# Optimization experiments

Measured on AMD Instinct MI355X. Metric: run time of the kernel, lower is better.

## Reference

```python
import jax, jax.numpy as jnp
import numpy as np

N_FIELDS = 26
VOCAB = 100000
EMBED = 16
BATCH = 16384
K = 16
N = N_FIELDS * EMBED  # 416


def setup_inputs() -> dict:
    key = jax.random.key(0)
    k1, k2, k3, k4, k5 = jax.random.split(key, 5)
    X = jax.random.randint(k1, (BATCH, N_FIELDS), 0, VOCAB, dtype=jnp.int64)
    tables = jax.random.normal(k2, (N_FIELDS, VOCAB, EMBED), dtype=jnp.float32) * 0.01
    W = jax.random.normal(k3, (N, 1), dtype=jnp.float32) * 0.05
    b = jax.random.normal(k4, (1,), dtype=jnp.float32)
    v = jax.random.normal(k5, (N, K), dtype=jnp.float32) * 0.05
    return {"X": X, "tables": tables, "W": W, "b": b, "v": v}


def reference(X, tables, W, b, v):
    # per-field gather: tables[f, X[:, f]] -> [B, F, E]
    emb = jax.vmap(lambda t, idx: t[idx], in_axes=(0, 1), out_axes=1)(tables, X)
    all_emb = emb.reshape(emb.shape[0], -1)  # [B, n] concat over fields
    linear_part = all_emb @ W + b  # [B, 1]
    xv = all_emb @ v               # [B, k]
    square_of_sum = xv * xv
    sum_of_square = (all_emb * all_emb) @ (v * v)
    interaction = 0.5 * jnp.sum(square_of_sum - sum_of_square, axis=-1, keepdims=True)
    return jax.nn.sigmoid(linear_part + interaction)
```

## Files before the change

kernel.cpp:

```cpp
#include <hip/hip_runtime.h>
#include <math.h>

#define NF 26
#define VOCAB 100000
#define EMB 16
#define BATCH 16384
#define KD 16
#define NTOT (NF * EMB)
#define VSTRIDE 20

__global__ __launch_bounds__(256, 4) void fm_kernel(
    const int* __restrict__ X, const float* __restrict__ tables,
    const float* __restrict__ W, const float* __restrict__ bptr,
    const float* __restrict__ v, float* __restrict__ out) {
    __shared__ float vL[NTOT * VSTRIDE];
    __shared__ float2 wvs[NTOT];

    const int tid = threadIdx.x;

    for (int t = tid; t < NTOT * KD; t += 256) {
        int n = t >> 4, k = t & 15;
        vL[n * VSTRIDE + k] = v[t];
    }
    for (int n = tid; n < NTOT; n += 256) {
        const float* vr = v + n * KD;
        float s = 0.f;
#pragma unroll
        for (int k = 0; k < KD; ++k) s = fmaf(vr[k], vr[k], s);
        wvs[n] = make_float2(W[n], s);
    }
    __syncthreads();

    const int g = tid >> 4;
    const int j = tid & 15;
    const int row = blockIdx.x * 16 + g;

    int idx[NF];
    {
        const int2* xr = (const int2*)(X + row * NF);
#pragma unroll
        for (int i = 0; i < NF / 2; ++i) {
            int2 t2 = xr[i];
            idx[2 * i] = t2.x;
            idx[2 * i + 1] = t2.y;
        }
    }

    float e[NF];
#pragma unroll
    for (int f = 0; f < NF; ++f) {
        unsigned off =
            (unsigned)(f * VOCAB + idx[f]) * (unsigned)(EMB * 4) + (j << 2);
        e[f] = *(const float*)((const char*)tables + off);
    }

    float xv[KD];
#pragma unroll
    for (int k = 0; k < KD; ++k) xv[k] = 0.f;
    float lin = 0.f, sos = 0.f;

#pragma unroll
    for (int f = 0; f < NF; ++f) {
        const int n = f * EMB + j;
        const float4* vr = (const float4*)&vL[n * VSTRIDE];
        float4 v0 = vr[0], v1 = vr[1], v2 = vr[2], v3 = vr[3];
        const float ef = e[f];
        xv[0] = fmaf(ef, v0.x, xv[0]);
        xv[1] = fmaf(ef, v0.y, xv[1]);
        xv[2] = fmaf(ef, v0.z, xv[2]);
        xv[3] = fmaf(ef, v0.w, xv[3]);
        xv[4] = fmaf(ef, v1.x, xv[4]);
        xv[5] = fmaf(ef, v1.y, xv[5]);
        xv[6] = fmaf(ef, v1.z, xv[6]);
        xv[7] = fmaf(ef, v1.w, xv[7]);
        xv[8] = fmaf(ef, v2.x, xv[8]);
        xv[9] = fmaf(ef, v2.y, xv[9]);
        xv[10] = fmaf(ef, v2.z, xv[10]);
        xv[11] = fmaf(ef, v2.w, xv[11]);
        xv[12] = fmaf(ef, v3.x, xv[12]);
        xv[13] = fmaf(ef, v3.y, xv[13]);
        xv[14] = fmaf(ef, v3.z, xv[14]);
        xv[15] = fmaf(ef, v3.w, xv[15]);

        float2 w2 = wvs[n];
        lin = fmaf(ef, w2.x, lin);
        sos = fmaf(ef * ef, w2.y, sos);
    }

#pragma unroll
    for (int m = 1; m < 16; m <<= 1) {
#pragma unroll
        for (int k = 0; k < KD; ++k) xv[k] += __shfl_xor(xv[k], m, 16);
    }

    float ss = 0.f;
#pragma unroll
    for (int k = 0; k < KD; ++k) ss = fmaf(xv[k], xv[k], ss);

    float t = fmaf(-0.5f, sos, lin);
#pragma unroll
    for (int m = 1; m < 16; m <<= 1) t += __shfl_xor(t, m, 16);

    if (j == 0) {
        const float z = t + 0.5f * ss + bptr[0];
        out[row] = 1.0f / (1.0f + __expf(-z));
    }
}

extern "C" void kernel_launch(void* const* d_in, const int* in_sizes, int n_in,
                              void* d_out, int out_size, void* d_ws,
                              size_t ws_size, hipStream_t stream) {
    const int* X = (const int*)d_in[0];
    const float* tables = (const float*)d_in[1];
    const float* W = (const float*)d_in[2];
    const float* b = (const float*)d_in[3];
    const float* v = (const float*)d_in[4];
    float* out = (float*)d_out;

    fm_kernel<<<BATCH / 16, 256, 0, stream>>>(X, tables, W, b, v, out);
}
```

Before: 220.0 us.

## Compute FM interaction projection with bf16 MFMA on 8-row single-wave blocks

Replaces the per-thread scalar FMA accumulation of all_emb @ v with a bf16 16x16x32 MFMA per field pair. Each 64-thread block handles 8 rows, with lanes loading 32-byte vector chunks of embeddings. v is loaded straight from global into per-lane B fragments instead of being staged in shared memory. The linear and sum-of-squares terms are fused into one nested FMA with a pre-negated coefficient. This cuts ALU work and shared-memory traffic, but rounds the embeddings and v to bf16 and half of the MFMA tile rows are wasted duplicates.

```diff
diff --git a/kernel.cpp b/kernel.cpp
--- a/kernel.cpp
+++ b/kernel.cpp
@@ -1,109 +1,132 @@
 #include <hip/hip_runtime.h>
+#include <hip/hip_bf16.h>
 #include <math.h>
 
 #define NF 26
 #define VOCAB 100000
 #define EMB 16
 #define BATCH 16384
-#define KD 16
-#define NTOT (NF * EMB)
-#define VSTRIDE 20
+#define NTOT 416
+#define NCHUNK 13
+#define RPB 8
 
-__global__ __launch_bounds__(256, 4) void fm_kernel(
+typedef __attribute__((ext_vector_type(8))) short bf16x8;
+typedef __attribute__((ext_vector_type(4))) float f32x4;
+
+__device__ __forceinline__ short2 cvt_pk(float a, float b) {
+    union { __hip_bfloat162 h; short2 s; } u;
+    u.h = __float22bfloat162_rn(make_float2(a, b));
+    return u.s;
+}
+
+__device__ __forceinline__ bf16x8 pack8(float4 a, float4 b) {
+    short2 p0 = cvt_pk(a.x, a.y), p1 = cvt_pk(a.z, a.w);
+    short2 p2 = cvt_pk(b.x, b.y), p3 = cvt_pk(b.z, b.w);
+    bf16x8 r;
+    r[0] = p0.x; r[1] = p0.y; r[2] = p1.x; r[3] = p1.y;
+    r[4] = p2.x; r[5] = p2.y; r[6] = p3.x; r[7] = p3.y;
+    return r;
+}
+
+__global__ __launch_bounds__(64, 2) void fm_kernel(
     const int* __restrict__ X, const float* __restrict__ tables,
     const float* __restrict__ W, const float* __restrict__ bptr,
     const float* __restrict__ v, float* __restrict__ out) {
-    __shared__ float vL[NTOT * VSTRIDE];
     __shared__ float2 wvs[NTOT];
 
-    const int tid = threadIdx.x;
+    const int l = threadIdx.x;
+    const int col = l & 15;
+    const int quad = l >> 4;
+    const int halfsel = quad & 1;
+    const int fpar = quad >> 1;
+    const int r = blockIdx.x * RPB + (col & 7);
 
-    for (int t = tid; t < NTOT * KD; t += 256) {
-        int n = t >> 4, k = t & 15;
-        vL[n * VSTRIDE + k] = v[t];
+    int idxv[NCHUNK];
+    {
+        const int* xr = X + r * NF + fpar;
+#pragma unroll
+        for (int c = 0; c < NCHUNK; ++c) idxv[c] = xr[2 * c];
     }
-    for (int n = tid; n < NTOT; n += 256) {
-        const float* vr = v + n * KD;
-        float s = 0.f;
+
+    for (int n = l; n < NTOT; n += 64) {
+        const float4* vr = (const float4*)(v + n * 16);
+        float4 a0 = vr[0], a1 = vr[1], a2 = vr[2], a3 = vr[3];
+        float s = a0.x * a0.x;
+        s = fmaf(a0.y, a0.y, s); s = fmaf(a0.z, a0.z, s); s = fmaf(a0.w, a0.w, s);
+        s = fmaf(a1.x, a1.x, s); s = fmaf(a1.y, a1.y, s); s = fmaf(a1.z, a1.z, s);
+        s = fmaf(a1.w, a1.w, s); s = fmaf(a2.x, a2.x, s); s = fmaf(a2.y, a2.y, s);
+        s = fmaf(a2.z, a2.z, s); s = fmaf(a2.w, a2.w, s); s = fmaf(a3.x, a3.x, s);
+        s = fmaf(a3.y, a3.y, s); s = fmaf(a3.z, a3.z, s); s = fmaf(a3.w, a3.w, s);
+        wvs[n] = make_float2(W[n], -0.5f * s);
+    }
+
+    bf16x8 Bf[NCHUNK];
 #pragma unroll
-        for (int k = 0; k < KD; ++k) s = fmaf(vr[k], vr[k], s);
-        wvs[n] = make_float2(W[n], s);
+    for (int c = 0; c < NCHUNK; ++c) {
+        const float* vp = v + (c * 32 + quad * 8) * 16 + col;
+        float4 b0 = make_float4(vp[0], vp[16], vp[32], vp[48]);
+        float4 b1 = make_float4(vp[64], vp[80], vp[96], vp[112]);
+        Bf[c] = pack8(b0, b1);
     }
+
     __syncthreads();
 
-    const int g = tid >> 4;
-    const int j = tid & 15;
-    const int row = blockIdx.x * 16 + g;
-
-    int idx[NF];
-    {
-        const int2* xr = (const int2*)(X + row * NF);
+    float4 g0[NCHUNK], g1[NCHUNK];
 #pragma unroll
-        for (int i = 0; i < NF / 2; ++i) {
-            int2 t2 = xr[i];
-            idx[2 * i] = t2.x;
-            idx[2 * i + 1] = t2.y;
-        }
+    for (int c = 0; c < NCHUNK; ++c) {
+        const int f = 2 * c + fpar;
+        const char* base = (const char*)tables +
+                           (((unsigned)(f * VOCAB + idxv[c])) << 6) +
+                           (halfsel << 5);
+        g0[c] = *(const float4*)base;
+        g1[c] = *(const float4*)(base + 16);
     }
 
-    float e[NF];
+    f32x4 acc = {0.f, 0.f, 0.f, 0.f};
+    float tp = 0.f;
 #pragma unroll
-    for (int f = 0; f < NF; ++f) {
-        unsigned off =
-            (unsigned)(f * VOCAB + idx[f]) * (unsigned)(EMB * 4) + (j << 2);
-        e[f] = *(const float*)((const char*)tables + off);
+    for (int c = 0; c < NCHUNK; ++c) {
+        float4 e0 = g0[c], e1 = g1[c];
+        const float4* wp = (const float4*)&wvs[c * 32 + quad * 8];
+        float4 w0 = wp[0], w1 = wp[1], w2 = wp[2], w3 = wp[3];
+        tp = fmaf(e0.x, fmaf(e0.x, w0.y, w0.x), tp);
+        tp = fmaf(e0.y, fmaf(e0.y, w0.w, w0.z), tp);
+        tp = fmaf(e0.z, fmaf(e0.z, w1.y, w1.x), tp);
+        tp = fmaf(e0.w, fmaf(e0.w, w1.w, w1.z), tp);
+        tp = fmaf(e1.x, fmaf(e1.x, w2.y, w2.x), tp);
+        tp = fmaf(e1.y, fmaf(e1.y, w2.w, w2.z), tp);
+        tp = fmaf(e1.z, fmaf(e1.z, w3.y, w3.x), tp);
+        tp = fmaf(e1.w, fmaf(e1.w, w3.w, w3.z), tp);
+        acc = __builtin_amdgcn_mfma_f32_16x16x32_bf16(pack8(e0, e1), Bf[c],
+                                                      acc, 0, 0, 0);
     }
 
-    float xv[KD];
+    tp += __shfl_xor(tp, 16);
+    tp += __shfl_xor(tp, 32);
+
+    float s0 = acc[0] * acc[0], s1 = acc[1] * acc[1];
+    float s2 = acc[2] * acc[2], s3 = acc[3] * acc[3];
 #pragma unroll
-    for (int k = 0; k < KD; ++k) xv[k] = 0.f;
-    float lin = 0.f, sos = 0.f;
-
-#pragma unroll
-    for (int f = 0; f < NF; ++f) {
-        const int n = f * EMB + j;
-        const float4* vr = (const float4*)&vL[n * VSTRIDE];
-        float4 v0 = vr[0], v1 = vr[1], v2 = vr[2], v3 = vr[3];
-        const float ef = e[f];
-        xv[0] = fmaf(ef, v0.x, xv[0]);
-        xv[1] = fmaf(ef, v0.y, xv[1]);
-        xv[2] = fmaf(ef, v0.z, xv[2]);
-        xv[3] = fmaf(ef, v0.w, xv[3]);
-        xv[4] = fmaf(ef, v1.x, xv[4]);
-        xv[5] = fmaf(ef, v1.y, xv[5]);
-        xv[6] = fmaf(ef, v1.z, xv[6]);
-        xv[7] = fmaf(ef, v1.w, xv[7]);
-        xv[8] = fmaf(ef, v2.x, xv[8]);
-        xv[9] = fmaf(ef, v2.y, xv[9]);
-        xv[10] = fmaf(ef, v2.z, xv[10]);
-        xv[11] = fmaf(ef, v2.w, xv[11]);
-        xv[12] = fmaf(ef, v3.x, xv[12]);
-        xv[13] = fmaf(ef, v3.y, xv[13]);
-        xv[14] = fmaf(ef, v3.z, xv[14]);
-        xv[15] = fmaf(ef, v3.w, xv[15]);
-
-        float2 w2 = wvs[n];
-        lin = fmaf(ef, w2.x, lin);
-        sos = fmaf(ef * ef, w2.y, sos);
+    for (int mask = 1; mask < 16; mask <<= 1) {
+        s0 += __shfl_xor(s0, mask);
+        s1 += __shfl_xor(s1, mask);
+        s2 += __shfl_xor(s2, mask);
+        s3 += __shfl_xor(s3, mask);
     }
 
-#pragma unroll
-    for (int m = 1; m < 16; m <<= 1) {
-#pragma unroll
-        for (int k = 0; k < KD; ++k) xv[k] += __shfl_xor(xv[k], m, 16);
-    }
+    float t0 = __shfl(tp, quad * 4 + 0);
+    float t1 = __shfl(tp, quad * 4 + 1);
+    float t2 = __shfl(tp, quad * 4 + 2);
+    float t3 = __shfl(tp, quad * 4 + 3);
 
-    float ss = 0.f;
-#pragma unroll
-    for (int k = 0; k < KD; ++k) ss = fmaf(xv[k], xv[k], ss);
-
-    float t = fmaf(-0.5f, sos, lin);
-#pragma unroll
-    for (int m = 1; m < 16; m <<= 1) t += __shfl_xor(t, m, 16);
-
-    if (j == 0) {
-        const float z = t + 0.5f * ss + bptr[0];
-        out[row] = 1.0f / (1.0f + __expf(-z));
+    if (col == 0 && quad < 2) {
+        const float bb = bptr[0];
+        float4 o;
+        o.x = 1.f / (1.f + __expf(-(t0 + 0.5f * s0 + bb)));
+        o.y = 1.f / (1.f + __expf(-(t1 + 0.5f * s1 + bb)));
+        o.z = 1.f / (1.f + __expf(-(t2 + 0.5f * s2 + bb)));
+        o.w = 1.f / (1.f + __expf(-(t3 + 0.5f * s3 + bb)));
+        *(float4*)(out + blockIdx.x * RPB + quad * 4) = o;
     }
 }
 
@@ -117,5 +140,5 @@
     const float* v = (const float*)d_in[4];
     float* out = (float*)d_out;
 
-    fm_kernel<<<BATCH / 16, 256, 0, stream>>>(X, tables, W, b, v, out);
+    fm_kernel<<<BATCH / RPB, 64, 0, stream>>>(X, tables, W, b, v, out);
 }
```

After: 219.2 us. About the same (-0.4%).
